# Performance work log

Hardware: AMD Instinct MI355X
Metric: run time of the kernel (lower is better)

## Reference

```python
import jax, jax.numpy as jnp
import numpy as np

B, T, I, H, N = 32, 512, 128, 128, 16  # batch, time, input, hidden_per_rnn, num_rnn


def setup_inputs() -> dict:
    key = jax.random.key(0)
    k1, k2, k3 = jax.random.split(key, 3)
    x = jax.random.normal(k1, (B, T, I), dtype=jnp.float32)
    # scale weights like torch RNN default init (uniform ~ 1/sqrt(Htot)) to keep relu recurrence stable
    s = 1.0 / np.sqrt(H * N)
    W_ih = jax.random.normal(k2, (H * N, I), dtype=jnp.float32) * s
    W_hh = jax.random.normal(k3, (H * N, H * N), dtype=jnp.float32) * s
    b_ih = jnp.zeros((H * N,), dtype=jnp.float32)
    b_hh = jnp.zeros((H * N,), dtype=jnp.float32)
    return {"x": x, "W_ih": W_ih, "W_hh": W_hh, "b_ih": b_ih, "b_hh": b_hh, "num_rnn": N}


def reference(x, W_ih, W_hh, b_ih, b_hh, num_rnn):
    Bq, Tq, _ = x.shape
    Htot = W_hh.shape[0]
    n = int(num_rnn)
    h = Htot // n
    # block-diagonal mask: keep only the n diagonal (h x h) blocks of W_hh
    idx = jnp.arange(n)
    blocks = W_hh.reshape(n, h, n, h)[idx, :, idx, :]  # (n, h, h)
    # input projection + biases done once outside the recurrence
    pre = jnp.einsum('bti,hi->bth', x, W_ih) + b_ih + b_hh  # (B, T, Htot)
    pre = pre.reshape(Bq, Tq, n, h).transpose(1, 0, 2, 3)  # (T, B, n, h)

    def step(hprev, p):
        # h_t = relu(pre_t + h_{t-1} @ W_block^T) per independent block
        hnew = jax.nn.relu(p + jnp.einsum('bnh,ngh->bng', hprev, blocks))
        return hnew, hnew

    h0 = jnp.zeros((Bq, n, h), dtype=x.dtype)
    _, hs = jax.lax.scan(step, h0, pre)  # (T, B, n, h)
    hs_all = hs.transpose(1, 0, 2, 3)  # (B, T, num_rnn, hidden_size)
    hidden = hs_all[:, -1].reshape(Bq, n * h)[None]  # (1, B, Htot), detached in torch
    hidden = jax.lax.stop_gradient(hidden)
    return hs_all, hidden
```

## Files before the change

### kernel.cpp

```cpp
#include <hip/hip_runtime.h>
#include <hip/hip_bf16.h>

#define BB   32
#define TT   512
#define II   128
#define HH   128
#define NR   16
#define HTOT 2048

typedef __attribute__((ext_vector_type(8))) short short8;
typedef __attribute__((ext_vector_type(4))) float f32x4;

static __device__ __forceinline__ short f2bf(float f) {
    union { __hip_bfloat16 h; short s; } u;
    u.h = __float2bfloat16(f);
    return u.s;
}
static __device__ __forceinline__ float bf2f(unsigned short u) {
    return __uint_as_float(((unsigned int)u) << 16);
}

__global__ __launch_bounds__(512, 2) void msml_pre(
    const float* __restrict__ x,
    const float* __restrict__ Wih,
    const float* __restrict__ bih,
    const float* __restrict__ bhh,
    unsigned short* __restrict__ pre)
{
    const int mx = blockIdx.x;
    const int n  = blockIdx.y;
    const int tid = threadIdx.x;
    const int w = tid >> 6, l = tid & 63;
    const int q = l >> 4;
    const int r0 = mx * 128;
    const int b  = r0 >> 9;
    const int t0 = r0 & 511;
    const int g  = b >> 4, m = b & 15;

    __shared__ short A[128 * 136];

    {
        const int row = tid >> 2, cb = tid & 3;
        const float4* xs = reinterpret_cast<const float4*>(x + (size_t)(r0 + row) * II + cb * 32);
        short* dst = &A[row * 136 + cb * 32];
#pragma unroll
        for (int i = 0; i < 8; ++i) {
            float4 v = xs[i];
            *reinterpret_cast<short4*>(dst + 4 * i) =
                make_short4(f2bf(v.x), f2bf(v.y), f2bf(v.z), f2bf(v.w));
        }
    }

    const int j = w * 16 + (l & 15);
    short8 bw[4];
    {
        const float* wb = Wih + (size_t)(n * HH + j) * II + q * 8;
#pragma unroll
        for (int kt = 0; kt < 4; ++kt) {
            float4 u0 = *reinterpret_cast<const float4*>(wb + kt * 32);
            float4 u1 = *reinterpret_cast<const float4*>(wb + kt * 32 + 4);
            short8 s;
            s[0] = f2bf(u0.x); s[1] = f2bf(u0.y); s[2] = f2bf(u0.z); s[3] = f2bf(u0.w);
            s[4] = f2bf(u1.x); s[5] = f2bf(u1.y); s[6] = f2bf(u1.z); s[7] = f2bf(u1.w);
            bw[kt] = s;
        }
    }
    const float bias = bih[n * HH + j] + bhh[n * HH + j];
    __syncthreads();

    const size_t ng = (size_t)(n * 2 + g);
#pragma unroll
    for (int mt = 0; mt < 8; ++mt) {
        const short* ap = &A[(mt * 16 + (l & 15)) * 136 + q * 8];
        f32x4 acc = {0.f, 0.f, 0.f, 0.f};
#pragma unroll
        for (int kt = 0; kt < 4; ++kt) {
            short8 a = *reinterpret_cast<const short8*>(ap + kt * 32);
            acc = __builtin_amdgcn_mfma_f32_16x16x32_bf16(a, bw[kt], acc, 0, 0, 0);
        }
#pragma unroll
        for (int r = 0; r < 4; ++r) {
            const int t = t0 + mt * 16 + q * 4 + r;
            pre[((ng * TT + t) * 16 + m) * 128 + j] = (unsigned short)f2bf(acc[r] + bias);
        }
    }
}

__global__ __launch_bounds__(512, 2) void msml_recur(
    const float* __restrict__ Whh,
    const unsigned short* __restrict__ pre,
    float* __restrict__ out)
{
    const int n = blockIdx.x;
    const int g = blockIdx.y;
    const int tid = threadIdx.x;
    const int w = tid >> 6, l = tid & 63;
    const int q = l >> 4;
    const int j = w * 16 + (l & 15);

    __shared__ short Hl[2][16 * 136];

    short8 bw[4];
    {
        const float* wb = Whh + (size_t)(n * HH + j) * HTOT + n * HH + q * 8;
#pragma unroll
        for (int kt = 0; kt < 4; ++kt) {
            float4 u0 = *reinterpret_cast<const float4*>(wb + kt * 32);
            float4 u1 = *reinterpret_cast<const float4*>(wb + kt * 32 + 4);
            short8 s;
            s[0] = f2bf(u0.x); s[1] = f2bf(u0.y); s[2] = f2bf(u0.z); s[3] = f2bf(u0.w);
            s[4] = f2bf(u1.x); s[5] = f2bf(u1.y); s[6] = f2bf(u1.z); s[7] = f2bf(u1.w);
            bw[kt] = s;
        }
    }

    for (int i = tid; i < 16 * 136; i += 512) Hl[0][i] = 0;

    const unsigned short* pb = pre + ((size_t)(n * 2 + g) * TT) * 2048 + (q * 4) * 128 + j;
    unsigned short pA0, pA1, pA2, pA3, pB0, pB1, pB2, pB3;
    { const unsigned short* pp = pb;        pA0 = pp[0]; pA1 = pp[128]; pA2 = pp[256]; pA3 = pp[384]; }
    { const unsigned short* pp = pb + 2048; pB0 = pp[0]; pB1 = pp[128]; pB2 = pp[256]; pB3 = pp[384]; }

    const size_t MS = (size_t)TT * HTOT;
    float* ob = out + (size_t)(g * 16 + q * 4) * MS + n * HH + j;

    __syncthreads();

#define RSTEP(HRD, HWR, P0, P1, P2, P3, TCUR)                                      \
    {                                                                              \
        const short* hp = &HRD[(l & 15) * 136 + q * 8];                            \
        f32x4 acc = {0.f, 0.f, 0.f, 0.f};                                          \
        _Pragma("unroll")                                                          \
        for (int kt = 0; kt < 4; ++kt) {                                           \
            short8 a = *reinterpret_cast<const short8*>(hp + kt * 32);             \
            acc = __builtin_amdgcn_mfma_f32_16x16x32_bf16(a, bw[kt], acc, 0, 0, 0);\
        }                                                                          \
        float h0 = fmaxf(acc[0] + bf2f(P0), 0.f);                                  \
        float h1 = fmaxf(acc[1] + bf2f(P1), 0.f);                                  \
        float h2 = fmaxf(acc[2] + bf2f(P2), 0.f);                                  \
        float h3 = fmaxf(acc[3] + bf2f(P3), 0.f);                                  \
        { int tn = (TCUR) + 2 < TT ? (TCUR) + 2 : TT - 1;                          \
          const unsigned short* pp = pb + (size_t)tn * 2048;                       \
          P0 = pp[0]; P1 = pp[128]; P2 = pp[256]; P3 = pp[384]; }                  \
        float* oo = ob + (size_t)(TCUR) * HTOT;                                    \
        oo[0] = h0; oo[MS] = h1; oo[2 * MS] = h2; oo[3 * MS] = h3;                 \
        HWR[(q * 4 + 0) * 136 + j] = f2bf(h0);                                     \
        HWR[(q * 4 + 1) * 136 + j] = f2bf(h1);                                     \
        HWR[(q * 4 + 2) * 136 + j] = f2bf(h2);                                     \
        HWR[(q * 4 + 3) * 136 + j] = f2bf(h3);                                     \
        if ((TCUR) == TT - 1) {                                                    \
            float* hh = out + (size_t)BB * TT * HTOT                               \
                        + (size_t)(g * 16 + q * 4) * HTOT + n * HH + j;            \
            hh[0] = h0; hh[HTOT] = h1; hh[2 * HTOT] = h2; hh[3 * HTOT] = h3;       \
        }                                                                          \
        __syncthreads();                                                           \
    }

    short* hb0 = &Hl[0][0];
    short* hb1 = &Hl[1][0];
    for (int t = 0; t < TT; t += 2) {
        RSTEP(hb0, hb1, pA0, pA1, pA2, pA3, t)
        RSTEP(hb1, hb0, pB0, pB1, pB2, pB3, t + 1)
    }
#undef RSTEP
}

__global__ __launch_bounds__(512, 4) void msml_fused2(
    const float* __restrict__ x,
    const float* __restrict__ Wih,
    const float* __restrict__ Whh,
    const float* __restrict__ bih,
    const float* __restrict__ bhh,
    float* __restrict__ out)
{
    const int n    = blockIdx.x;
    const int b    = blockIdx.y;
    const int tid  = threadIdx.x;
    const int wave = tid >> 6;
    const int lane = tid & 63;
    const int s    = lane >> 4;
    const int j    = wave * 16 + (lane & 15);
    const int row  = n * HH + j;

    float wih[32], whh[32];
    {
        const float4* wi4 = reinterpret_cast<const float4*>(Wih + (size_t)row * II);
        const float4* wh4 = reinterpret_cast<const float4*>(Whh + (size_t)row * HTOT + n * HH);
#pragma unroll
        for (int k = 0; k < 8; ++k) {
            float4 a = wi4[4 * k + s];
            wih[4*k+0] = a.x; wih[4*k+1] = a.y; wih[4*k+2] = a.z; wih[4*k+3] = a.w;
            float4 c = wh4[4 * k + s];
            whh[4*k+0] = c.x; whh[4*k+1] = c.y; whh[4*k+2] = c.z; whh[4*k+3] = c.w;
        }
    }
    const float bias0 = (s == 0) ? (bih[row] + bhh[row]) : 0.0f;

    __shared__ float hs[2][HH];
    if (tid < HH) hs[0][tid] = 0.0f;

    const float* xrow = x + (size_t)b * TT * II;
    float* orow = out + (size_t)b * TT * HTOT + (size_t)n * HH + j;

    float accx;
    {
        const float4* xv = reinterpret_cast<const float4*>(xrow);
        float a0 = bias0, a1 = 0.f, a2 = 0.f, a3 = 0.f;
#pragma unroll
        for (int k = 0; k < 8; ++k) {
            float4 v = xv[4 * k + s];
            a0 += wih[4*k+0] * v.x; a1 += wih[4*k+1] * v.y;
            a2 += wih[4*k+2] * v.z; a3 += wih[4*k+3] * v.w;
        }
        accx = (a0 + a1) + (a2 + a3);
    }
    __syncthreads();

    float hn = 0.0f;
    int buf = 0;
    for (int t = 0; t < TT; ++t) {
        float4 xn[8];
        if (t + 1 < TT) {
            const float4* xv = reinterpret_cast<const float4*>(xrow + (size_t)(t + 1) * II);
#pragma unroll
            for (int k = 0; k < 8; ++k) xn[k] = xv[4 * k + s];
        }
        const float4* hv = reinterpret_cast<const float4*>(hs[buf]);
        float a0 = accx, a1 = 0.f, a2 = 0.f, a3 = 0.f;
#pragma unroll
        for (int k = 0; k < 8; ++k) {
            float4 v = hv[4 * k + s];
            a0 += whh[4*k+0] * v.x; a1 += whh[4*k+1] * v.y;
            a2 += whh[4*k+2] * v.z; a3 += whh[4*k+3] * v.w;
        }
        float sum = (a0 + a1) + (a2 + a3);
        sum += __shfl_xor(sum, 16);
        sum += __shfl_xor(sum, 32);
        hn = fmaxf(sum, 0.0f);

        if (s == 0) {
            orow[(size_t)t * HTOT] = hn;
            hs[buf ^ 1][j] = hn;
        }
        {
            float b0 = bias0, b1 = 0.f, b2 = 0.f, b3 = 0.f;
#pragma unroll
            for (int k = 0; k < 8; ++k) {
                b0 += wih[4*k+0] * xn[k].x; b1 += wih[4*k+1] * xn[k].y;
                b2 += wih[4*k+2] * xn[k].z; b3 += wih[4*k+3] * xn[k].w;
            }
            accx = (b0 + b1) + (b2 + b3);
        }
        buf ^= 1;
        __syncthreads();
    }

    if (s == 0)
        out[(size_t)BB * TT * HTOT + (size_t)b * HTOT + row] = hn;
}

extern "C" void kernel_launch(void* const* d_in, const int* in_sizes, int n_in,
                              void* d_out, int out_size, void* d_ws, size_t ws_size,
                              hipStream_t stream) {
    const float* x   = (const float*)d_in[0];
    const float* Wih = (const float*)d_in[1];
    const float* Whh = (const float*)d_in[2];
    const float* bih = (const float*)d_in[3];
    const float* bhh = (const float*)d_in[4];
    float* out = (float*)d_out;

    const size_t pre_bytes = (size_t)NR * 2 * TT * 16 * 128 * sizeof(unsigned short);

    if (ws_size >= pre_bytes && d_ws != nullptr) {
        unsigned short* pre = (unsigned short*)d_ws;
        msml_pre<<<dim3(128, NR), 512, 0, stream>>>(x, Wih, bih, bhh, pre);
        msml_recur<<<dim3(NR, 2), 512, 0, stream>>>(Whh, pre, out);
    } else {
        msml_fused2<<<dim3(NR, BB), 512, 0, stream>>>(x, Wih, Whh, bih, bhh, out);
    }
}
```

Baseline: 211.4 us.

## Run recurrence in a single wavefront per block to drop barriers

```diff
diff --git a/kernel.cpp b/kernel.cpp
--- a/kernel.cpp
+++ b/kernel.cpp
@@ -15,9 +15,6 @@
     union { __hip_bfloat16 h; short s; } u;
     u.h = __float2bfloat16(f);
     return u.s;
-}
-static __device__ __forceinline__ float bf2f(unsigned short u) {
-    return __uint_as_float(((unsigned int)u) << 16);
 }
 
 __global__ __launch_bounds__(512, 2) void msml_pre(
@@ -86,83 +83,97 @@
     }
 }
 
-__global__ __launch_bounds__(512, 2) void msml_recur(
+__global__ __launch_bounds__(64, 1) void msml_recur1w(
     const float* __restrict__ Whh,
     const unsigned short* __restrict__ pre,
     float* __restrict__ out)
 {
     const int n = blockIdx.x;
     const int g = blockIdx.y;
-    const int tid = threadIdx.x;
-    const int w = tid >> 6, l = tid & 63;
+    const int l = threadIdx.x;
+    const int m = l & 15;
     const int q = l >> 4;
-    const int j = w * 16 + (l & 15);
-
-    __shared__ short Hl[2][16 * 136];
-
-    short8 bw[4];
-    {
-        const float* wb = Whh + (size_t)(n * HH + j) * HTOT + n * HH + q * 8;
+
+    __shared__ short Hs[16 * 136];
+
+    short8 wf[8][4];
+#pragma unroll
+    for (int it = 0; it < 8; ++it)
 #pragma unroll
         for (int kt = 0; kt < 4; ++kt) {
-            float4 u0 = *reinterpret_cast<const float4*>(wb + kt * 32);
-            float4 u1 = *reinterpret_cast<const float4*>(wb + kt * 32 + 4);
+            const float* wp = Whh + (size_t)(n * HH + it * 16 + m) * HTOT + n * HH + kt * 32 + q * 8;
+            float4 u0 = *reinterpret_cast<const float4*>(wp);
+            float4 u1 = *reinterpret_cast<const float4*>(wp + 4);
             short8 s;
             s[0] = f2bf(u0.x); s[1] = f2bf(u0.y); s[2] = f2bf(u0.z); s[3] = f2bf(u0.w);
             s[4] = f2bf(u1.x); s[5] = f2bf(u1.y); s[6] = f2bf(u1.z); s[7] = f2bf(u1.w);
-            bw[kt] = s;
-        }
-    }
-
-    for (int i = tid; i < 16 * 136; i += 512) Hl[0][i] = 0;
-
-    const unsigned short* pb = pre + ((size_t)(n * 2 + g) * TT) * 2048 + (q * 4) * 128 + j;
-    unsigned short pA0, pA1, pA2, pA3, pB0, pB1, pB2, pB3;
-    { const unsigned short* pp = pb;        pA0 = pp[0]; pA1 = pp[128]; pA2 = pp[256]; pA3 = pp[384]; }
-    { const unsigned short* pp = pb + 2048; pB0 = pp[0]; pB1 = pp[128]; pB2 = pp[256]; pB3 = pp[384]; }
-
-    const size_t MS = (size_t)TT * HTOT;
-    float* ob = out + (size_t)(g * 16 + q * 4) * MS + n * HH + j;
-
-    __syncthreads();
-
-#define RSTEP(HRD, HWR, P0, P1, P2, P3, TCUR)                                      \
-    {                                                                              \
-        const short* hp = &HRD[(l & 15) * 136 + q * 8];                            \
-        f32x4 acc = {0.f, 0.f, 0.f, 0.f};                                          \
-        _Pragma("unroll")                                                          \
-        for (int kt = 0; kt < 4; ++kt) {                                           \
-            short8 a = *reinterpret_cast<const short8*>(hp + kt * 32);             \
-            acc = __builtin_amdgcn_mfma_f32_16x16x32_bf16(a, bw[kt], acc, 0, 0, 0);\
-        }                                                                          \
-        float h0 = fmaxf(acc[0] + bf2f(P0), 0.f);                                  \
-        float h1 = fmaxf(acc[1] + bf2f(P1), 0.f);                                  \
-        float h2 = fmaxf(acc[2] + bf2f(P2), 0.f);                                  \
-        float h3 = fmaxf(acc[3] + bf2f(P3), 0.f);                                  \
-        { int tn = (TCUR) + 2 < TT ? (TCUR) + 2 : TT - 1;                          \
-          const unsigned short* pp = pb + (size_t)tn * 2048;                       \
-          P0 = pp[0]; P1 = pp[128]; P2 = pp[256]; P3 = pp[384]; }                  \
-        float* oo = ob + (size_t)(TCUR) * HTOT;                                    \
-        oo[0] = h0; oo[MS] = h1; oo[2 * MS] = h2; oo[3 * MS] = h3;                 \
-        HWR[(q * 4 + 0) * 136 + j] = f2bf(h0);                                     \
-        HWR[(q * 4 + 1) * 136 + j] = f2bf(h1);                                     \
-        HWR[(q * 4 + 2) * 136 + j] = f2bf(h2);                                     \
-        HWR[(q * 4 + 3) * 136 + j] = f2bf(h3);                                     \
-        if ((TCUR) == TT - 1) {                                                    \
-            float* hh = out + (size_t)BB * TT * HTOT                               \
-                        + (size_t)(g * 16 + q * 4) * HTOT + n * HH + j;            \
-            hh[0] = h0; hh[HTOT] = h1; hh[2 * HTOT] = h2; hh[3 * HTOT] = h3;       \
-        }                                                                          \
-        __syncthreads();                                                           \
-    }
-
-    short* hb0 = &Hl[0][0];
-    short* hb1 = &Hl[1][0];
-    for (int t = 0; t < TT; t += 2) {
-        RSTEP(hb0, hb1, pA0, pA1, pA2, pA3, t)
-        RSTEP(hb1, hb0, pB0, pB1, pB2, pB3, t + 1)
-    }
-#undef RSTEP
+            wf[it][kt] = s;
+        }
+
+    short8 aid;
+#pragma unroll
+    for (int e = 0; e < 8; ++e) aid[e] = (q * 8 + e == m) ? (short)0x3F80 : (short)0;
+
+    const short8 zs = {0, 0, 0, 0, 0, 0, 0, 0};
+    const f32x4 zero4 = {0.f, 0.f, 0.f, 0.f};
+
+    const unsigned short* pb = pre + (size_t)(n * 2 + g) * TT * 2048 + m * 128;
+    float* ob = out + (size_t)(g * 16 + m) * TT * HTOT + n * HH;
+
+    f32x4 acc[8];
+#pragma unroll
+    for (int it = 0; it < 8; ++it) {
+        short8 pf = (q < 2) ? *reinterpret_cast<const short8*>(pb + it * 16 + q * 8) : zs;
+        acc[it] = __builtin_amdgcn_mfma_f32_16x16x32_bf16(aid, pf, zero4, 0, 0, 0);
+    }
+    short8 hf[4];
+#pragma unroll
+    for (int kt = 0; kt < 4; ++kt) hf[kt] = zs;
+
+    for (int t = 0; t < TT; ++t) {
+        const bool last = (t == TT - 1);
+
+        short8 pn[8];
+        if (!last) {
+            const unsigned short* pp = pb + (size_t)(t + 1) * 2048;
+#pragma unroll
+            for (int it = 0; it < 8; ++it)
+                pn[it] = (q < 2) ? *reinterpret_cast<const short8*>(pp + it * 16 + q * 8) : zs;
+        }
+
+#pragma unroll
+        for (int kt = 0; kt < 4; ++kt)
+#pragma unroll
+            for (int it = 0; it < 8; ++it)
+                acc[it] = __builtin_amdgcn_mfma_f32_16x16x32_bf16(wf[it][kt], hf[kt], acc[it], 0, 0, 0);
+
+#pragma unroll
+        for (int it = 0; it < 8; ++it) {
+            float h0 = fmaxf(acc[it][0], 0.f);
+            float h1 = fmaxf(acc[it][1], 0.f);
+            float h2 = fmaxf(acc[it][2], 0.f);
+            float h3 = fmaxf(acc[it][3], 0.f);
+            unsigned int p0 = (unsigned int)(unsigned short)f2bf(h0) |
+                              ((unsigned int)(unsigned short)f2bf(h1) << 16);
+            unsigned int p1 = (unsigned int)(unsigned short)f2bf(h2) |
+                              ((unsigned int)(unsigned short)f2bf(h3) << 16);
+            *reinterpret_cast<uint2*>(&Hs[m * 136 + it * 16 + q * 4]) = make_uint2(p0, p1);
+            float4 hv = make_float4(h0, h1, h2, h3);
+            *reinterpret_cast<float4*>(ob + (size_t)t * HTOT + it * 16 + q * 4) = hv;
+            if (last)
+                *reinterpret_cast<float4*>(out + (size_t)BB * TT * HTOT +
+                                           (size_t)(g * 16 + m) * HTOT + n * HH + it * 16 + q * 4) = hv;
+        }
+
+        if (!last) {
+#pragma unroll
+            for (int kt = 0; kt < 4; ++kt)
+                hf[kt] = *reinterpret_cast<const short8*>(&Hs[m * 136 + kt * 32 + q * 8]);
+#pragma unroll
+            for (int it = 0; it < 8; ++it)
+                acc[it] = __builtin_amdgcn_mfma_f32_16x16x32_bf16(aid, pn[it], zero4, 0, 0, 0);
+        }
+    }
 }
 
 __global__ __launch_bounds__(512, 4) void msml_fused2(
@@ -274,7 +285,7 @@
     if (ws_size >= pre_bytes && d_ws != nullptr) {
         unsigned short* pre = (unsigned short*)d_ws;
         msml_pre<<<dim3(128, NR), 512, 0, stream>>>(x, Wih, bih, bhh, pre);
-        msml_recur<<<dim3(NR, 2), 512, 0, stream>>>(Whh, pre, out);
+        msml_recur1w<<<dim3(NR, 2), 64, 0, stream>>>(Whh, pre, out);
     } else {
         msml_fused2<<<dim3(NR, BB), 512, 0, stream>>>(x, Wih, Whh, bih, bhh, out);
     }
```

After: 445.3 us. 2.11x slower.
